# Optimization experiments

Hardware: AMD Instinct MI355X
Metric: run time of the kernel (lower is better)

## Reference

```python
import jax, jax.numpy as jnp
import numpy as np

KS = 3      # kernel_size
PAD = 1     # padding
GROUPS = 4

def _patches(a, H, W):
    # a: [B, C, H+2*PAD, W+2*PAD] -> [B, C, H, W, KS, KS]
    return jnp.stack([
        jnp.stack([a[:, :, i:i + H, j:j + W] for j in range(KS)], axis=-1)
        for i in range(KS)], axis=-2)

def setup_inputs() -> dict:
    key = jax.random.key(0)
    ks = jax.random.split(key, 7)
    B, Cin, Cout, H, W = 8, 256, 256, 64, 64
    std = np.sqrt(2.0 / Cout)  # kaiming fan_out
    return {
        "x": jax.random.normal(ks[0], (B, Cin, H, W), jnp.float32),
        "y": jax.random.normal(ks[1], (B, Cin, H, W), jnp.float32),
        "wq": jax.random.normal(ks[2], (Cout, Cin), jnp.float32) * std,
        "wk": jax.random.normal(ks[3], (Cout, Cin), jnp.float32) * std,
        "wv": jax.random.normal(ks[4], (Cout, Cin), jnp.float32) * std,
        "rel_h": jax.random.normal(ks[5], (Cout // 2, 1, 1, KS, 1), jnp.float32),
        "rel_w": jax.random.normal(ks[6], (Cout // 2, 1, 1, 1, KS), jnp.float32),
    }

def reference(x, y, wq, wk, wv, rel_h, rel_w):
    B, _, H, W = x.shape
    Cout = wq.shape[0]
    half = Cout // 2
    xp = jnp.pad(x, ((0, 0), (0, 0), (PAD, PAD), (PAD, PAD)))
    q = jnp.einsum('oi,bihw->bohw', wq, y)          # [B,Cout,H,W]
    k = jnp.einsum('oi,bihw->bohw', wk, xp)         # [B,Cout,H+2,W+2]
    v = jnp.einsum('oi,bihw->bohw', wv, xp)
    kp = _patches(k, H, W)                          # [B,Cout,H,W,KS,KS]
    vp = _patches(v, H, W)
    kp = jnp.concatenate([kp[:, :half] + rel_h[None], kp[:, half:] + rel_w[None]], axis=1)
    cg = Cout // GROUPS
    kp = kp.reshape(B, GROUPS, cg, H, W, KS * KS)
    vp = vp.reshape(B, GROUPS, cg, H, W, KS * KS)
    qg = q.reshape(B, GROUPS, cg, H, W, 1)
    attn = jax.nn.softmax(qg * kp, axis=-1)         # per-channel softmax over window
    out = jnp.einsum('bnchwk,bnchwk->bnchw', attn, vp)
    return out.reshape(B, Cout, H, W)
```

## Files before the change

kernel.cpp:

```cpp
#include <hip/hip_runtime.h>
#include <hip/hip_bf16.h>
#include <stdint.h>

typedef __attribute__((ext_vector_type(8))) short short8;
typedef __attribute__((ext_vector_type(4))) float floatx4;
typedef __attribute__((ext_vector_type(4))) unsigned int uintx4;
typedef __attribute__((ext_vector_type(2))) unsigned int uintx2;
typedef unsigned int u32;

#define HH 64
#define WW 64
#define HWSZ 4096
#define BB 8
#define CIN 256
#define COUT 256
#define NTOT 32768

#define GLL16(g, l)                                                            \
    __builtin_amdgcn_global_load_lds(                                          \
        (const __attribute__((address_space(1))) u32*)(const void*)(g),        \
        (__attribute__((address_space(3))) u32*)(void*)(l), 16, 0, 0)

__device__ __forceinline__ unsigned short f2b(float f) {
    union { float f; unsigned int u; } v; v.f = f;
    unsigned int r = v.u + 0x7FFFu + ((v.u >> 16) & 1u);
    return (unsigned short)(r >> 16);
}
__device__ __forceinline__ float b2f(unsigned short h) {
    union { unsigned int u; float f; } v; v.u = ((unsigned int)h) << 16;
    return v.f;
}
__device__ __forceinline__ unsigned int pk2(float lo, float hi) {
    unsigned int r;
    asm("v_cvt_pk_bf16_f32 %0, %1, %2" : "=v"(r) : "v"(lo), "v"(hi));
    return r;
}

__global__ void wcast(const float* __restrict__ wq, const float* __restrict__ wk,
                      const float* __restrict__ wv,
                      unsigned short* __restrict__ wqb, unsigned short* __restrict__ wkb,
                      unsigned short* __restrict__ wvb) {
    int idx = blockIdx.x * 256 + threadIdx.x;
    wqb[idx] = f2b(wq[idx]);
    wkb[idx] = f2b(wk[idx]);
    wvb[idx] = f2b(wv[idx]);
}

__global__ __launch_bounds__(256)
void gemm_qkv(const unsigned short* __restrict__ wqb, const unsigned short* __restrict__ wkb,
              const unsigned short* __restrict__ wvb,
              const float* __restrict__ xf, const float* __restrict__ yf,
              unsigned short* __restrict__ Qb, unsigned short* __restrict__ Kb,
              unsigned short* __restrict__ Vb) {
    __shared__ unsigned short lA[2][128 * 32];
    __shared__ unsigned short lB[2][128 * 32];

    int d = blockIdx.x;
    int X = d & 7;
    int kk = d >> 3;
    int g = kk / 6;
    int j = kk - g * 6;
    int n_tile = g * 8 + X;
    int z = j >> 1;
    int m0 = (j & 1) * 128;
    int n0 = n_tile * 128;

    const unsigned short* Wb = (z == 0) ? wqb : (z == 1) ? wkb : wvb;
    const float* In = (z == 0) ? yf : xf;
    unsigned short* Out = (z == 0) ? Qb : (z == 1) ? Kb : Vb;

    int bb = n0 >> 12;
    int p0 = n0 & 4095;
    int t = threadIdx.x;
    int lane = t & 63;
    int wave = t >> 6;
    int quad = lane >> 4;
    int l16 = lane & 15;
    int wm = (wave >> 1) * 64;
    int wn = (wave & 1) * 64;

    int rA = t >> 2;
    int qA = t & 3;
    int cchA = 8 * (qA ^ ((rA >> 1) & 3));
    const unsigned short* gA0 = Wb + (size_t)(m0 + rA) * CIN + cchA;
    const unsigned short* gA1 = gA0 + (size_t)64 * CIN;

    int sbase = t & 31;
    int ng = sbase * 4;
    int kq = (t >> 5) * 4;
    const float* gB = In + ((size_t)bb * CIN + kq) * HWSZ + p0 + ng;
    int wr_idx[4];
    #pragma unroll
    for (int jj = 0; jj < 4; ++jj) {
        int s = jj * 32 + sbase;
        wr_idx[jj] = s * 32 + (((kq >> 3) ^ ((s >> 1) & 3)) << 3) + (kq & 4);
    }

    int swzA = (l16 >> 1) & 3;
    int rBr = (wn >> 2) + l16;
    int swzB = (rBr >> 1) & 3;
    int rdA = (wm + l16) * 32 + ((quad ^ swzA) << 3);
    int rdB = rBr * 32 + ((quad ^ swzB) << 3);

    floatx4 acc[4][4];
    #pragma unroll
    for (int mi = 0; mi < 4; ++mi)
        #pragma unroll
        for (int ni = 0; ni < 4; ++ni)
            acc[mi][ni] = (floatx4){0.f, 0.f, 0.f, 0.f};

    floatx4 bl[2][4];

    #pragma unroll
    for (int i = 0; i < 4; ++i)
        bl[0][i] = *(const floatx4*)(gB + (size_t)i * HWSZ);
    __builtin_amdgcn_sched_barrier(0);
    GLL16(gA0, lA[0] + wave * 512);
    GLL16(gA1, lA[0] + wave * 512 + 2048);
    __builtin_amdgcn_sched_barrier(0);
    #pragma unroll
    for (int i = 0; i < 4; ++i)
        bl[1][i] = *(const floatx4*)(gB + (size_t)(32 + i) * HWSZ);
    asm volatile("s_waitcnt vmcnt(6)" ::: "memory");
    #pragma unroll
    for (int jj = 0; jj < 4; ++jj) {
        unsigned int d0 = pk2(bl[0][0][jj], bl[0][1][jj]);
        unsigned int d1 = pk2(bl[0][2][jj], bl[0][3][jj]);
        *(uintx2*)(lB[0] + wr_idx[jj]) = (uintx2){d0, d1};
    }
    asm volatile("s_waitcnt vmcnt(4) lgkmcnt(0)" ::: "memory");
    __builtin_amdgcn_s_barrier();
    __builtin_amdgcn_sched_barrier(0);

    #pragma unroll
    for (int it = 0; it < 8; ++it) {
        if (it < 7) {
            GLL16(gA0 + (it + 1) * 32, lA[(it + 1) & 1] + wave * 512);
            GLL16(gA1 + (it + 1) * 32, lA[(it + 1) & 1] + wave * 512 + 2048);
        }
        __builtin_amdgcn_sched_barrier(0);
        if (it < 6) {
            #pragma unroll
            for (int i = 0; i < 4; ++i)
                bl[it & 1][i] = *(const floatx4*)(gB + (size_t)((it + 2) * 32 + i) * HWSZ);
        }

        short8 af[4], bf[4];
        #pragma unroll
        for (int mi = 0; mi < 4; ++mi)
            af[mi] = *(const short8*)(lA[it & 1] + rdA + mi * 512);
        #pragma unroll
        for (int ni = 0; ni < 4; ++ni)
            bf[ni] = *(const short8*)(lB[it & 1] + rdB + ni * 1024);
        #pragma unroll
        for (int mi = 0; mi < 4; ++mi)
            #pragma unroll
            for (int ni = 0; ni < 4; ++ni)
                acc[mi][ni] = __builtin_amdgcn_mfma_f32_16x16x32_bf16(af[mi], bf[ni], acc[mi][ni], 0, 0, 0);

        if (it < 7) {
            if (it < 6) { asm volatile("s_waitcnt vmcnt(6)" ::: "memory"); }
            else        { asm volatile("s_waitcnt vmcnt(2)" ::: "memory"); }
            #pragma unroll
            for (int jj = 0; jj < 4; ++jj) {
                unsigned int d0 = pk2(bl[(it + 1) & 1][0][jj], bl[(it + 1) & 1][1][jj]);
                unsigned int d1 = pk2(bl[(it + 1) & 1][2][jj], bl[(it + 1) & 1][3][jj]);
                *(uintx2*)(lB[(it + 1) & 1] + wr_idx[jj]) = (uintx2){d0, d1};
            }
            if (it < 6) { asm volatile("s_waitcnt vmcnt(4) lgkmcnt(0)" ::: "memory"); }
            else        { asm volatile("s_waitcnt vmcnt(0) lgkmcnt(0)" ::: "memory"); }
            __builtin_amdgcn_s_barrier();
            __builtin_amdgcn_sched_barrier(0);
        }
    }

    int colb = n0 + wn + 4 * l16;
    #pragma unroll
    for (int mi = 0; mi < 4; ++mi) {
        #pragma unroll
        for (int r = 0; r < 4; ++r) {
            int row = m0 + wm + mi * 16 + quad * 4 + r;
            unsigned int lo = (unsigned int)f2b(acc[mi][0][r]) | ((unsigned int)f2b(acc[mi][1][r]) << 16);
            unsigned int hi = (unsigned int)f2b(acc[mi][2][r]) | ((unsigned int)f2b(acc[mi][3][r]) << 16);
            *(uintx2*)(Out + (size_t)row * NTOT + colb) = (uintx2){lo, hi};
        }
    }
}

__global__ __launch_bounds__(256)
void attn(const unsigned short* __restrict__ Q,
          const unsigned short* __restrict__ K,
          const unsigned short* __restrict__ V,
          const float* __restrict__ rel_h,
          const float* __restrict__ rel_w,
          float* __restrict__ out) {
    int gid = blockIdx.x * 256 + threadIdx.x;
    int w8 = gid & 7;
    int w0 = w8 << 3;
    int h = (gid >> 3) & 63;
    int c = (gid >> 9) & 255;
    int b = gid >> 17;

    size_t nb = (size_t)c * NTOT + (size_t)b * HWSZ;
    const unsigned short* Kp = K + nb;
    const unsigned short* Vp = V + nb;

    short8 qr = *(const short8*)(Q + nb + h * 64 + w0);

    bool use_h = (c < 128);
    float rel3[3];
    if (use_h) {
        rel3[0] = rel_h[c * 3 + 0]; rel3[1] = rel_h[c * 3 + 1]; rel3[2] = rel_h[c * 3 + 2];
    } else {
        int cc = c - 128;
        rel3[0] = rel_w[cc * 3 + 0]; rel3[1] = rel_w[cc * 3 + 1]; rel3[2] = rel_w[cc * 3 + 2];
    }
    float rr[9];
    #pragma unroll
    for (int r = 0; r < 3; ++r)
        #pragma unroll
        for (int j = 0; j < 3; ++j)
            rr[r * 3 + j] = use_h ? rel3[r] : rel3[j];

    int e0 = (w0 > 0) ? w0 - 1 : 0;
    int e9 = (w0 < 56) ? w0 + 8 : 63;
    bool okL = (w0 > 0);
    bool okR = (w0 < 56);

    float kb[3][10], vb[3][10];
    #pragma unroll
    for (int r = 0; r < 3; ++r) {
        int ihr = h + r - 1;
        bool rok = (unsigned)ihr < 64u;
        int ihc = ihr < 0 ? 0 : (ihr > 63 ? 63 : ihr);
        int ro = ihc * 64;
        short8 km = *(const short8*)(Kp + ro + w0);
        short8 vm = *(const short8*)(Vp + ro + w0);
        float ke0 = b2f(Kp[ro + e0]), ve0 = b2f(Vp[ro + e0]);
        float ke9 = b2f(Kp[ro + e9]), ve9 = b2f(Vp[ro + e9]);
        #pragma unroll
        for (int i = 0; i < 8; ++i) {
            kb[r][i + 1] = rok ? b2f((unsigned short)km[i]) : 0.f;
            vb[r][i + 1] = rok ? b2f((unsigned short)vm[i]) : 0.f;
        }
        bool ok0 = rok && okL;
        bool ok9 = rok && okR;
        kb[r][0] = ok0 ? ke0 : 0.f;  vb[r][0] = ok0 ? ve0 : 0.f;
        kb[r][9] = ok9 ? ke9 : 0.f;  vb[r][9] = ok9 ? ve9 : 0.f;
    }

    float q[8];
    #pragma unroll
    for (int i = 0; i < 8; ++i) q[i] = b2f((unsigned short)qr[i]);

    float ov[8];
    #pragma unroll
    for (int wi = 0; wi < 8; ++wi) {
        float qv = q[wi];
        float lg[9];
        #pragma unroll
        for (int r = 0; r < 3; ++r)
            #pragma unroll
            for (int j = 0; j < 3; ++j)
                lg[r * 3 + j] = qv * (kb[r][wi + j] + rr[r * 3 + j]);
        float m = lg[0];
        #pragma unroll
        for (int t2 = 1; t2 < 9; ++t2) m = fmaxf(m, lg[t2]);
        float s = 0.f, o = 0.f;
        #pragma unroll
        for (int r = 0; r < 3; ++r)
            #pragma unroll
            for (int j = 0; j < 3; ++j) {
                float e = __expf(lg[r * 3 + j] - m);
                s += e;
                o += e * vb[r][wi + j];
            }
        ov[wi] = o * __builtin_amdgcn_rcpf(s);
    }

    size_t oi = ((size_t)b * COUT + c) * HWSZ + h * 64 + w0;
    *(floatx4*)(out + oi)     = (floatx4){ ov[0], ov[1], ov[2], ov[3] };
    *(floatx4*)(out + oi + 4) = (floatx4){ ov[4], ov[5], ov[6], ov[7] };
}

extern "C" void kernel_launch(void* const* d_in, const int* in_sizes, int n_in,
                              void* d_out, int out_size, void* d_ws, size_t ws_size,
                              hipStream_t stream) {
    const float* x = (const float*)d_in[0];
    const float* y = (const float*)d_in[1];
    const float* wq = (const float*)d_in[2];
    const float* wk = (const float*)d_in[3];
    const float* wv = (const float*)d_in[4];
    const float* rel_h = (const float*)d_in[5];
    const float* rel_w = (const float*)d_in[6];
    float* out = (float*)d_out;

    char* ws = (char*)d_ws;
    unsigned short* wqb = (unsigned short*)(ws + 33554432);
    unsigned short* wkb = (unsigned short*)(ws + 33554432 + 131072);
    unsigned short* wvb = (unsigned short*)(ws + 33554432 + 262144);
    unsigned short* Qb  = (unsigned short*)(ws + 33947648);
    unsigned short* Kb  = (unsigned short*)(ws + 33947648 + 16777216);
    unsigned short* Vb  = (unsigned short*)(ws + 33947648 + 33554432);

    wcast<<<256, 256, 0, stream>>>(wq, wk, wv, wqb, wkb, wvb);
    gemm_qkv<<<1536, 256, 0, stream>>>(wqb, wkb, wvb, x, y, Qb, Kb, Vb);
    attn<<<4096, 256, 0, stream>>>(Qb, Kb, Vb, rel_h, rel_w, out);
}
```

Baseline: 158.1 us.

## Stage full-K input tile in LDS once and reuse across both M halves

The QKV GEMM now loads and converts the whole 128-column by 256-deep fp32 input tile to bf16 in a 64KB swizzled LDS buffer once per block, then computes both 128-row output halves from it. Weight fragments are read straight from global memory instead of through LDS. This halves the number of blocks and removes the duplicate fp32 input reads and conversions that came from splitting M across two blocks. The cost is lost load/compute pipelining, since all loads finish before any MFMA, and lower occupancy from the larger LDS footprint.

```diff
diff --git a/kernel.cpp b/kernel.cpp
--- a/kernel.cpp
+++ b/kernel.cpp
@@ -15,11 +15,6 @@
 #define CIN 256
 #define COUT 256
 #define NTOT 32768
-
-#define GLL16(g, l)                                                            \
-    __builtin_amdgcn_global_load_lds(                                          \
-        (const __attribute__((address_space(1))) u32*)(const void*)(g),        \
-        (__attribute__((address_space(3))) u32*)(void*)(l), 16, 0, 0)
 
 __device__ __forceinline__ unsigned short f2b(float f) {
     union { float f; unsigned int u; } v; v.f = f;
@@ -52,17 +47,14 @@
               const float* __restrict__ xf, const float* __restrict__ yf,
               unsigned short* __restrict__ Qb, unsigned short* __restrict__ Kb,
               unsigned short* __restrict__ Vb) {
-    __shared__ unsigned short lA[2][128 * 32];
-    __shared__ unsigned short lB[2][128 * 32];
+    __shared__ unsigned char lB[65536];
 
     int d = blockIdx.x;
     int X = d & 7;
     int kk = d >> 3;
-    int g = kk / 6;
-    int j = kk - g * 6;
+    int g = kk / 3;
+    int z = kk - g * 3;
     int n_tile = g * 8 + X;
-    int z = j >> 1;
-    int m0 = (j & 1) * 128;
     int n0 = n_tile * 128;
 
     const unsigned short* Wb = (z == 0) ? wqb : (z == 1) ? wkb : wvb;
@@ -79,110 +71,75 @@
     int wm = (wave >> 1) * 64;
     int wn = (wave & 1) * 64;
 
-    int rA = t >> 2;
-    int qA = t & 3;
-    int cchA = 8 * (qA ^ ((rA >> 1) & 3));
-    const unsigned short* gA0 = Wb + (size_t)(m0 + rA) * CIN + cchA;
-    const unsigned short* gA1 = gA0 + (size_t)64 * CIN;
-
-    int sbase = t & 31;
-    int ng = sbase * 4;
-    int kq = (t >> 5) * 4;
-    const float* gB = In + ((size_t)bb * CIN + kq) * HWSZ + p0 + ng;
-    int wr_idx[4];
+    int sb = t & 31;
+    int kq0 = (t >> 5) * 4;
+    int kq0h = kq0 >> 3;
+    int kq0b = (kq0 & 4) * 2;
+    const float* gB = In + ((size_t)bb * CIN + kq0) * HWSZ + p0 + 4 * sb;
+    int sxor[4], sboff[4];
     #pragma unroll
     for (int jj = 0; jj < 4; ++jj) {
-        int s = jj * 32 + sbase;
-        wr_idx[jj] = s * 32 + (((kq >> 3) ^ ((s >> 1) & 3)) << 3) + (kq & 4);
-    }
-
-    int swzA = (l16 >> 1) & 3;
+        int s = jj * 32 + sb;
+        sxor[jj] = s & 31;
+        sboff[jj] = s * 512 + kq0b;
+    }
+
+    #pragma unroll
+    for (int c = 0; c < 8; ++c) {
+        floatx4 v[4];
+        #pragma unroll
+        for (int i = 0; i < 4; ++i)
+            v[i] = *(const floatx4*)(gB + (size_t)(c * 32 + i) * HWSZ);
+        int gk = c * 4 + kq0h;
+        #pragma unroll
+        for (int jj = 0; jj < 4; ++jj) {
+            unsigned int d0 = pk2(v[0][jj], v[1][jj]);
+            unsigned int d1 = pk2(v[2][jj], v[3][jj]);
+            *(uintx2*)(lB + sboff[jj] + ((gk ^ sxor[jj]) << 4)) = (uintx2){d0, d1};
+        }
+    }
+    __syncthreads();
+
     int rBr = (wn >> 2) + l16;
-    int swzB = (rBr >> 1) & 3;
-    int rdA = (wm + l16) * 32 + ((quad ^ swzA) << 3);
-    int rdB = rBr * 32 + ((quad ^ swzB) << 3);
-
-    floatx4 acc[4][4];
-    #pragma unroll
-    for (int mi = 0; mi < 4; ++mi)
-        #pragma unroll
-        for (int ni = 0; ni < 4; ++ni)
-            acc[mi][ni] = (floatx4){0.f, 0.f, 0.f, 0.f};
-
-    floatx4 bl[2][4];
-
-    #pragma unroll
-    for (int i = 0; i < 4; ++i)
-        bl[0][i] = *(const floatx4*)(gB + (size_t)i * HWSZ);
-    __builtin_amdgcn_sched_barrier(0);
-    GLL16(gA0, lA[0] + wave * 512);
-    GLL16(gA1, lA[0] + wave * 512 + 2048);
-    __builtin_amdgcn_sched_barrier(0);
-    #pragma unroll
-    for (int i = 0; i < 4; ++i)
-        bl[1][i] = *(const floatx4*)(gB + (size_t)(32 + i) * HWSZ);
-    asm volatile("s_waitcnt vmcnt(6)" ::: "memory");
-    #pragma unroll
-    for (int jj = 0; jj < 4; ++jj) {
-        unsigned int d0 = pk2(bl[0][0][jj], bl[0][1][jj]);
-        unsigned int d1 = pk2(bl[0][2][jj], bl[0][3][jj]);
-        *(uintx2*)(lB[0] + wr_idx[jj]) = (uintx2){d0, d1};
-    }
-    asm volatile("s_waitcnt vmcnt(4) lgkmcnt(0)" ::: "memory");
-    __builtin_amdgcn_s_barrier();
-    __builtin_amdgcn_sched_barrier(0);
-
-    #pragma unroll
-    for (int it = 0; it < 8; ++it) {
-        if (it < 7) {
-            GLL16(gA0 + (it + 1) * 32, lA[(it + 1) & 1] + wave * 512);
-            GLL16(gA1 + (it + 1) * 32, lA[(it + 1) & 1] + wave * 512 + 2048);
-        }
-        __builtin_amdgcn_sched_barrier(0);
-        if (it < 6) {
-            #pragma unroll
-            for (int i = 0; i < 4; ++i)
-                bl[it & 1][i] = *(const floatx4*)(gB + (size_t)((it + 2) * 32 + i) * HWSZ);
-        }
-
-        short8 af[4], bf[4];
+    #pragma unroll
+    for (int mp = 0; mp < 2; ++mp) {
+        int m0 = mp * 128;
+        floatx4 acc[4][4];
         #pragma unroll
         for (int mi = 0; mi < 4; ++mi)
-            af[mi] = *(const short8*)(lA[it & 1] + rdA + mi * 512);
-        #pragma unroll
-        for (int ni = 0; ni < 4; ++ni)
-            bf[ni] = *(const short8*)(lB[it & 1] + rdB + ni * 1024);
-        #pragma unroll
-        for (int mi = 0; mi < 4; ++mi)
             #pragma unroll
             for (int ni = 0; ni < 4; ++ni)
-                acc[mi][ni] = __builtin_amdgcn_mfma_f32_16x16x32_bf16(af[mi], bf[ni], acc[mi][ni], 0, 0, 0);
-
-        if (it < 7) {
-            if (it < 6) { asm volatile("s_waitcnt vmcnt(6)" ::: "memory"); }
-            else        { asm volatile("s_waitcnt vmcnt(2)" ::: "memory"); }
-            #pragma unroll
-            for (int jj = 0; jj < 4; ++jj) {
-                unsigned int d0 = pk2(bl[(it + 1) & 1][0][jj], bl[(it + 1) & 1][1][jj]);
-                unsigned int d1 = pk2(bl[(it + 1) & 1][2][jj], bl[(it + 1) & 1][3][jj]);
-                *(uintx2*)(lB[(it + 1) & 1] + wr_idx[jj]) = (uintx2){d0, d1};
+                acc[mi][ni] = (floatx4){0.f, 0.f, 0.f, 0.f};
+
+        #pragma unroll
+        for (int c = 0; c < 8; ++c) {
+            short8 af[4], bf[4];
+            #pragma unroll
+            for (int mi = 0; mi < 4; ++mi)
+                af[mi] = *(const short8*)(Wb + (size_t)(m0 + wm + mi * 16 + l16) * CIN
+                                          + c * 32 + quad * 8);
+            #pragma unroll
+            for (int ni = 0; ni < 4; ++ni) {
+                int r = rBr + ni * 32;
+                bf[ni] = *(const short8*)(lB + r * 512 + (((c * 4 + quad) ^ (r & 31)) << 4));
             }
-            if (it < 6) { asm volatile("s_waitcnt vmcnt(4) lgkmcnt(0)" ::: "memory"); }
-            else        { asm volatile("s_waitcnt vmcnt(0) lgkmcnt(0)" ::: "memory"); }
-            __builtin_amdgcn_s_barrier();
-            __builtin_amdgcn_sched_barrier(0);
-        }
-    }
-
-    int colb = n0 + wn + 4 * l16;
-    #pragma unroll
-    for (int mi = 0; mi < 4; ++mi) {
-        #pragma unroll
-        for (int r = 0; r < 4; ++r) {
-            int row = m0 + wm + mi * 16 + quad * 4 + r;
-            unsigned int lo = (unsigned int)f2b(acc[mi][0][r]) | ((unsigned int)f2b(acc[mi][1][r]) << 16);
-            unsigned int hi = (unsigned int)f2b(acc[mi][2][r]) | ((unsigned int)f2b(acc[mi][3][r]) << 16);
-            *(uintx2*)(Out + (size_t)row * NTOT + colb) = (uintx2){lo, hi};
+            #pragma unroll
+            for (int mi = 0; mi < 4; ++mi)
+                #pragma unroll
+                for (int ni = 0; ni < 4; ++ni)
+                    acc[mi][ni] = __builtin_amdgcn_mfma_f32_16x16x32_bf16(af[mi], bf[ni], acc[mi][ni], 0, 0, 0);
+        }
+
+        int colb = n0 + wn + 4 * l16;
+        #pragma unroll
+        for (int mi = 0; mi < 4; ++mi) {
+            #pragma unroll
+            for (int r = 0; r < 4; ++r) {
+                int row = m0 + wm + mi * 16 + quad * 4 + r;
+                unsigned int lo = (unsigned int)f2b(acc[mi][0][r]) | ((unsigned int)f2b(acc[mi][1][r]) << 16);
+                unsigned int hi = (unsigned int)f2b(acc[mi][2][r]) | ((unsigned int)f2b(acc[mi][3][r]) << 16);
+                *(uintx2*)(Out + (size_t)row * NTOT + colb) = (uintx2){lo, hi};
+            }
         }
     }
 }
@@ -304,6 +261,6 @@
     unsigned short* Vb  = (unsigned short*)(ws + 33947648 + 33554432);
 
     wcast<<<256, 256, 0, stream>>>(wq, wk, wv, wqb, wkb, wvb);
-    gemm_qkv<<<1536, 256, 0, stream>>>(wqb, wkb, wvb, x, y, Qb, Kb, Vb);
+    gemm_qkv<<<768, 256, 0, stream>>>(wqb, wkb, wvb, x, y, Qb, Kb, Vb);
     attn<<<4096, 256, 0, stream>>>(Qb, Kb, Vb, rel_h, rel_w, out);
 }
```

After: 179.2 us. 1.13x slower.

## Single-buffer A tile and shallower B prefetch to raise GEMM occupancy

Applied to the files above, without the earlier changes.

Cuts the QKV GEMM's A-operand LDS buffer from double to single buffering and its register prefetch of B from two stages to one. It adds a minimum-6-blocks occupancy hint and swaps the hand-tuned waitcnt/s_barrier sequence for __syncthreads with an extra barrier per iteration. The goal is more resident waves to hide latency through occupancy rather than explicit software pipelining. In exchange, global loads now overlap only with one iteration's MFMAs, and more barriers may stall.

```diff
diff --git a/kernel.cpp b/kernel.cpp
--- a/kernel.cpp
+++ b/kernel.cpp
@@ -46,13 +46,13 @@
     wvb[idx] = f2b(wv[idx]);
 }
 
-__global__ __launch_bounds__(256)
+__global__ __launch_bounds__(256, 6)
 void gemm_qkv(const unsigned short* __restrict__ wqb, const unsigned short* __restrict__ wkb,
               const unsigned short* __restrict__ wvb,
               const float* __restrict__ xf, const float* __restrict__ yf,
               unsigned short* __restrict__ Qb, unsigned short* __restrict__ Kb,
               unsigned short* __restrict__ Vb) {
-    __shared__ unsigned short lA[2][128 * 32];
+    __shared__ unsigned short lA[128 * 32];
     __shared__ unsigned short lB[2][128 * 32];
 
     int d = blockIdx.x;
@@ -109,49 +109,41 @@
         for (int ni = 0; ni < 4; ++ni)
             acc[mi][ni] = (floatx4){0.f, 0.f, 0.f, 0.f};
 
-    floatx4 bl[2][4];
+    floatx4 bl[4];
 
     #pragma unroll
     for (int i = 0; i < 4; ++i)
-        bl[0][i] = *(const floatx4*)(gB + (size_t)i * HWSZ);
-    __builtin_amdgcn_sched_barrier(0);
-    GLL16(gA0, lA[0] + wave * 512);
-    GLL16(gA1, lA[0] + wave * 512 + 2048);
-    __builtin_amdgcn_sched_barrier(0);
-    #pragma unroll
-    for (int i = 0; i < 4; ++i)
-        bl[1][i] = *(const floatx4*)(gB + (size_t)(32 + i) * HWSZ);
-    asm volatile("s_waitcnt vmcnt(6)" ::: "memory");
+        bl[i] = *(const floatx4*)(gB + (size_t)i * HWSZ);
+    GLL16(gA0, lA + wave * 512);
+    GLL16(gA1, lA + wave * 512 + 2048);
     #pragma unroll
     for (int jj = 0; jj < 4; ++jj) {
-        unsigned int d0 = pk2(bl[0][0][jj], bl[0][1][jj]);
-        unsigned int d1 = pk2(bl[0][2][jj], bl[0][3][jj]);
+        unsigned int d0 = pk2(bl[0][jj], bl[1][jj]);
+        unsigned int d1 = pk2(bl[2][jj], bl[3][jj]);
         *(uintx2*)(lB[0] + wr_idx[jj]) = (uintx2){d0, d1};
     }
-    asm volatile("s_waitcnt vmcnt(4) lgkmcnt(0)" ::: "memory");
-    __builtin_amdgcn_s_barrier();
-    __builtin_amdgcn_sched_barrier(0);
+    __syncthreads();
 
     #pragma unroll
     for (int it = 0; it < 8; ++it) {
-        if (it < 7) {
-            GLL16(gA0 + (it + 1) * 32, lA[(it + 1) & 1] + wave * 512);
-            GLL16(gA1 + (it + 1) * 32, lA[(it + 1) & 1] + wave * 512 + 2048);
-        }
-        __builtin_amdgcn_sched_barrier(0);
-        if (it < 6) {
-            #pragma unroll
-            for (int i = 0; i < 4; ++i)
-                bl[it & 1][i] = *(const floatx4*)(gB + (size_t)((it + 2) * 32 + i) * HWSZ);
-        }
-
         short8 af[4], bf[4];
         #pragma unroll
         for (int mi = 0; mi < 4; ++mi)
-            af[mi] = *(const short8*)(lA[it & 1] + rdA + mi * 512);
+            af[mi] = *(const short8*)(lA + rdA + mi * 512);
         #pragma unroll
         for (int ni = 0; ni < 4; ++ni)
             bf[ni] = *(const short8*)(lB[it & 1] + rdB + ni * 1024);
+        __syncthreads();
+
+        if (it < 7) {
+            GLL16(gA0 + (it + 1) * 32, lA + wave * 512);
+            GLL16(gA1 + (it + 1) * 32, lA + wave * 512 + 2048);
+            #pragma unroll
+            for (int i = 0; i < 4; ++i)
+                bl[i] = *(const floatx4*)(gB + (size_t)((it + 1) * 32 + i) * HWSZ);
+        }
+        __builtin_amdgcn_sched_barrier(0);
+
         #pragma unroll
         for (int mi = 0; mi < 4; ++mi)
             #pragma unroll
@@ -159,18 +151,13 @@
                 acc[mi][ni] = __builtin_amdgcn_mfma_f32_16x16x32_bf16(af[mi], bf[ni], acc[mi][ni], 0, 0, 0);
 
         if (it < 7) {
-            if (it < 6) { asm volatile("s_waitcnt vmcnt(6)" ::: "memory"); }
-            else        { asm volatile("s_waitcnt vmcnt(2)" ::: "memory"); }
             #pragma unroll
             for (int jj = 0; jj < 4; ++jj) {
-                unsigned int d0 = pk2(bl[(it + 1) & 1][0][jj], bl[(it + 1) & 1][1][jj]);
-                unsigned int d1 = pk2(bl[(it + 1) & 1][2][jj], bl[(it + 1) & 1][3][jj]);
+                unsigned int d0 = pk2(bl[0][jj], bl[1][jj]);
+                unsigned int d1 = pk2(bl[2][jj], bl[3][jj]);
                 *(uintx2*)(lB[(it + 1) & 1] + wr_idx[jj]) = (uintx2){d0, d1};
             }
-            if (it < 6) { asm volatile("s_waitcnt vmcnt(4) lgkmcnt(0)" ::: "memory"); }
-            else        { asm volatile("s_waitcnt vmcnt(0) lgkmcnt(0)" ::: "memory"); }
-            __builtin_amdgcn_s_barrier();
-            __builtin_amdgcn_sched_barrier(0);
+            __syncthreads();
         }
     }
 
```

Result: slower. 327.6 us (+107.2%).
